# Performance work log

Hardware: AMD Instinct MI355X
Metric: run time of the kernel (lower is better)

## Reference

```python
import jax, jax.numpy as jnp
import numpy as np

N_NODES = 50000
N_REL = 8
N_EDGES = 64000
D_IN = 128
D_OUT = 128


def setup_inputs() -> dict:
    key = jax.random.key(0)
    k1, k2, k3, k4 = jax.random.split(key, 4)
    features = jax.random.normal(k1, (N_NODES, D_IN), dtype=jnp.float32)
    W = jax.random.normal(k2, (N_REL, D_IN, D_OUT), dtype=jnp.float32) * 0.05
    b = jnp.zeros((N_REL, D_OUT), dtype=jnp.float32)
    src = jax.random.randint(k3, (N_REL, N_EDGES), 0, N_NODES, dtype=jnp.int64)
    dst = jax.random.randint(k4, (N_REL, N_EDGES), 0, N_NODES, dtype=jnp.int64)
    return {"features": features, "W": W, "b": b, "src": src, "dst": dst}


def reference(features, W, b, src, dst):
    # R-GCN layer: per-relation DGL GraphConv (norm='both', bias) summed over relations.
    N = features.shape[0]
    R = W.shape[0]
    out = jnp.zeros((N, W.shape[-1]), dtype=features.dtype)
    for r in range(R):  # fixed small relation count; edges fully vectorized
        s, d = src[r], dst[r]
        ones = jnp.ones(s.shape[0], dtype=features.dtype)
        out_deg = jnp.clip(jax.ops.segment_sum(ones, s, num_segments=N), 1.0)
        in_deg = jnp.clip(jax.ops.segment_sum(ones, d, num_segments=N), 1.0)
        # pre-scale source features by out_degree^-1/2, gather, aggregate to dst
        m = features * (out_deg ** -0.5)[:, None]          # [N, D_in]
        agg = jax.ops.segment_sum(m[s], d, num_segments=N)  # [N, D_in]
        # weight after aggregation (in_feats == out_feats path), then dst norm + bias
        rst = (agg @ W[r]) * (in_deg ** -0.5)[:, None] + b[r]
        out = out + rst  # HeteroGraphConv aggregate='sum'
    return out
```

## Files before the change

kernel.cpp:

```cpp
#include <hip/hip_runtime.h>

#define N_NODES 50000
#define N_REL 8
#define N_EDGES 64000
#define D 128
#define TROWS 32
#define NT 1563
#define CAP 128
#define SLABW 66
#define GRID 521

typedef __attribute__((ext_vector_type(8))) short short8;
typedef __attribute__((ext_vector_type(4))) float f32x4;

__device__ __forceinline__ unsigned short f2bf(float x) {
  unsigned int u = __float_as_uint(x);
  u += 0x7FFFu + ((u >> 16) & 1u);
  return (unsigned short)(u >> 16);
}
__device__ __forceinline__ float bflo(unsigned v) { return __uint_as_float(v << 16); }
__device__ __forceinline__ float bfhi(unsigned v) { return __uint_as_float(v & 0xFFFF0000u); }
__device__ __forceinline__ unsigned packbf(float x, float y) {
  return (unsigned)f2bf(x) | ((unsigned)f2bf(y) << 16);
}

__global__ __launch_bounds__(256) void setup_kernel(
    const int* __restrict__ src, const int* __restrict__ dst,
    const float* __restrict__ F, const float* __restrict__ W,
    const float* __restrict__ b, int* __restrict__ outc, int* __restrict__ inc,
    uint2* __restrict__ F16, unsigned short* __restrict__ Wt,
    float* __restrict__ bs) {
  int bid = blockIdx.x, t = threadIdx.x;
  if (bid < 2000) {
    int i = bid * 256 + t;
    int r = i / N_EDGES;
    atomicAdd(&outc[r * N_NODES + src[i]], 1);
    atomicAdd(&inc[r * N_NODES + dst[i]], 1);
  } else if (bid < 8250) {
    int i = (bid - 2000) * 256 + t;
    float4 v = ((const float4*)F)[i];
    uint2 o;
    o.x = packbf(v.x, v.y);
    o.y = packbf(v.z, v.w);
    F16[i] = o;
  } else {
    int i = (bid - 8250) * 256 + t;
    int r = i >> 14, rem = i & 16383, n = rem >> 7, k = rem & 127;
    Wt[i] = f2bf(W[(r << 14) + (k << 7) + n]);
    if (bid == 8250 && t < D) {
      float v = 0.f;
#pragma unroll
      for (int rr = 0; rr < N_REL; ++rr) v += b[rr * D + t];
      bs[t] = v;
    }
  }
}

__global__ __launch_bounds__(256) void bucket_kernel(
    const int* __restrict__ src, const int* __restrict__ dst,
    const int* __restrict__ outc, const int* __restrict__ inc,
    int* __restrict__ bcnt, int2* __restrict__ buckets) {
  int i = blockIdx.x * 256 + threadIdx.x;
  int r = i / N_EDGES;
  int s = src[i], d = dst[i];
  float c = rsqrtf(fmaxf((float)outc[r * N_NODES + s], 1.0f)) *
            rsqrtf(fmaxf((float)inc[r * N_NODES + d], 1.0f));
  int tile = d >> 5;
  int slot = atomicAdd(&bcnt[r * NT + tile], 1);
  if (slot < CAP)
    buckets[(size_t)(r * NT + tile) * CAP + slot] =
        make_int2(s | ((d & 31) << 17), __float_as_int(c));
}

__global__ __launch_bounds__(512, 2) void fused_kernel(
    const unsigned int* __restrict__ F16,
    const unsigned short* __restrict__ Wt,
    const int* __restrict__ bcnt,
    const int2* __restrict__ buckets,
    const float* __restrict__ bs,
    float* __restrict__ out) {
  __shared__ unsigned slabs[8][TROWS * SLABW];
  __shared__ int2 dlds[8][CAP];
  int tid = threadIdx.x;
  int lane = tid & 63;
  int w = __builtin_amdgcn_readfirstlane(tid >> 6);
  int l15 = lane & 15, g = lane >> 4;

  short8 bfr[8][4];
#pragma unroll
  for (int r = 0; r < 8; ++r)
#pragma unroll
    for (int ks = 0; ks < 4; ++ks)
      bfr[r][ks] = *(const short8*)&Wt[(size_t)r * D * D +
                                       (w * 16 + l15) * D + ks * 32 + g * 8];
  float bias = bs[w * 16 + l15];

#define RMW(dd, fv)                                           \
  {                                                           \
    int row_ = ((dd).x >> 17) & 31;                           \
    unsigned* p_ = &slabs[w][row_ * SLABW + lane];            \
    float c_ = __int_as_float((dd).y);                        \
    unsigned old_ = *p_;                                      \
    float vx_ = fmaf(c_, bflo(fv), bflo(old_));               \
    float vy_ = fmaf(c_, bfhi(fv), bfhi(old_));               \
    *p_ = packbf(vx_, vy_);                                   \
  }

  for (int t = blockIdx.x; t < NT; t += GRID) {
    __syncthreads();

    for (int i = lane; i < TROWS * SLABW; i += 64) slabs[w][i] = 0u;

    int n = min(bcnt[w * NT + t], CAP);
    const int2* bk = &buckets[(size_t)(w * NT + t) * CAP];
    if (lane < n) dlds[w][lane] = bk[lane];
    if (lane + 64 < n) dlds[w][lane + 64] = bk[lane + 64];

    int i = 0;
    for (; i + 4 <= n; i += 4) {
      int2 d0 = dlds[w][i], d1 = dlds[w][i + 1], d2 = dlds[w][i + 2],
           d3 = dlds[w][i + 3];
      unsigned f0 = F16[(unsigned)(d0.x & 0x1FFFF) * 64 + lane];
      unsigned f1 = F16[(unsigned)(d1.x & 0x1FFFF) * 64 + lane];
      unsigned f2 = F16[(unsigned)(d2.x & 0x1FFFF) * 64 + lane];
      unsigned f3 = F16[(unsigned)(d3.x & 0x1FFFF) * 64 + lane];
      RMW(d0, f0) RMW(d1, f1) RMW(d2, f2) RMW(d3, f3)
    }
    for (; i < n; ++i) {
      int2 dd = dlds[w][i];
      unsigned fv = F16[(unsigned)(dd.x & 0x1FFFF) * 64 + lane];
      RMW(dd, fv)
    }

    __syncthreads();

    f32x4 a0 = (f32x4){0.f, 0.f, 0.f, 0.f};
    f32x4 a1 = (f32x4){0.f, 0.f, 0.f, 0.f};
#pragma unroll
    for (int r = 0; r < 8; ++r) {
#pragma unroll
      for (int ks = 0; ks < 4; ++ks) {
        short8 A0 = *(const short8*)&slabs[r][l15 * SLABW + ks * 16 + g * 4];
        short8 A1 =
            *(const short8*)&slabs[r][(16 + l15) * SLABW + ks * 16 + g * 4];
        a0 = __builtin_amdgcn_mfma_f32_16x16x32_bf16(A0, bfr[r][ks], a0, 0, 0, 0);
        a1 = __builtin_amdgcn_mfma_f32_16x16x32_bf16(A1, bfr[r][ks], a1, 0, 0, 0);
      }
    }

    int t0 = t * TROWS;
    int col = w * 16 + l15;
#pragma unroll
    for (int q = 0; q < 4; ++q) {
      int row0 = t0 + g * 4 + q;
      if (row0 < N_NODES) out[(size_t)row0 * D + col] = a0[q] + bias;
      int row1 = t0 + 16 + g * 4 + q;
      if (row1 < N_NODES) out[(size_t)row1 * D + col] = a1[q] + bias;
    }
  }
#undef RMW
}

extern "C" void kernel_launch(void* const* d_in, const int* in_sizes, int n_in,
                              void* d_out, int out_size, void* d_ws, size_t ws_size,
                              hipStream_t stream) {
  const float* F = (const float*)d_in[0];
  const float* W = (const float*)d_in[1];
  const float* b = (const float*)d_in[2];
  const int* src = (const int*)d_in[3];
  const int* dst = (const int*)d_in[4];
  float* out = (float*)d_out;

  char* ws = (char*)d_ws;
  size_t o = 0;
  int* outc = (int*)(ws + o);  o += (size_t)N_REL * N_NODES * 4;
  int* inc = (int*)(ws + o);   o += (size_t)N_REL * N_NODES * 4;
  int* bcnt = (int*)(ws + o);  o += (size_t)N_REL * NT * 4;
  size_t zero_bytes = o;
  int2* buckets = (int2*)(ws + o);               o += (size_t)N_REL * NT * CAP * 8;
  unsigned int* F16 = (unsigned int*)(ws + o);   o += (size_t)N_NODES * 64 * 4;
  unsigned short* Wt = (unsigned short*)(ws + o); o += (size_t)N_REL * D * D * 2;
  float* bs = (float*)(ws + o);                  o += D * 4;

  hipMemsetAsync(outc, 0, zero_bytes, stream);
  setup_kernel<<<8762, 256, 0, stream>>>(src, dst, F, W, b, outc, inc,
                                         (uint2*)F16, Wt, bs);
  bucket_kernel<<<2000, 256, 0, stream>>>(src, dst, outc, inc, bcnt, buckets);
  fused_kernel<<<GRID, 512, 0, stream>>>(F16, Wt, bcnt, buckets, bs, out);
}
```

Before: 207.6 us.

## Merge memset, setup, bucket and fused kernels into one cooperative kernel

Replaces the memset plus three kernel launches with a single cooperative kernel that uses grid-wide syncs between the zeroing, degree counting and conversion, bucketing, and aggregate/GEMM phases. The goal is to remove launch gaps and per-kernel tail overhead. In exchange, the grid shrinks to 256 blocks, so the fused phase runs with fewer blocks and has to pay for grid.sync barriers and the cooperative launch. The Wt conversion covers exactly 131072 threads, which matches N_REL*D*D.

```diff
diff --git a/kernel.cpp b/kernel.cpp
--- a/kernel.cpp
+++ b/kernel.cpp
@@ -1,4 +1,7 @@
 #include <hip/hip_runtime.h>
+#include <hip/hip_cooperative_groups.h>
+
+namespace cg = cooperative_groups;
 
 #define N_NODES 50000
 #define N_REL 8
@@ -8,7 +11,8 @@
 #define NT 1563
 #define CAP 128
 #define SLABW 66
-#define GRID 521
+#define GRID 256
+#define NTHR (GRID * 512)
 
 typedef __attribute__((ext_vector_type(8))) short short8;
 typedef __attribute__((ext_vector_type(4))) float f32x4;
@@ -24,64 +28,59 @@
   return (unsigned)f2bf(x) | ((unsigned)f2bf(y) << 16);
 }
 
-__global__ __launch_bounds__(256) void setup_kernel(
+__global__ __launch_bounds__(512, 2) void mega_kernel(
     const int* __restrict__ src, const int* __restrict__ dst,
     const float* __restrict__ F, const float* __restrict__ W,
     const float* __restrict__ b, int* __restrict__ outc, int* __restrict__ inc,
-    uint2* __restrict__ F16, unsigned short* __restrict__ Wt,
-    float* __restrict__ bs) {
-  int bid = blockIdx.x, t = threadIdx.x;
-  if (bid < 2000) {
-    int i = bid * 256 + t;
-    int r = i / N_EDGES;
-    atomicAdd(&outc[r * N_NODES + src[i]], 1);
-    atomicAdd(&inc[r * N_NODES + dst[i]], 1);
-  } else if (bid < 8250) {
-    int i = (bid - 2000) * 256 + t;
-    float4 v = ((const float4*)F)[i];
-    uint2 o;
-    o.x = packbf(v.x, v.y);
-    o.y = packbf(v.z, v.w);
-    F16[i] = o;
-  } else {
-    int i = (bid - 8250) * 256 + t;
-    int r = i >> 14, rem = i & 16383, n = rem >> 7, k = rem & 127;
-    Wt[i] = f2bf(W[(r << 14) + (k << 7) + n]);
-    if (bid == 8250 && t < D) {
-      float v = 0.f;
-#pragma unroll
-      for (int rr = 0; rr < N_REL; ++rr) v += b[rr * D + t];
-      bs[t] = v;
-    }
-  }
-}
-
-__global__ __launch_bounds__(256) void bucket_kernel(
-    const int* __restrict__ src, const int* __restrict__ dst,
-    const int* __restrict__ outc, const int* __restrict__ inc,
-    int* __restrict__ bcnt, int2* __restrict__ buckets) {
-  int i = blockIdx.x * 256 + threadIdx.x;
-  int r = i / N_EDGES;
-  int s = src[i], d = dst[i];
-  float c = rsqrtf(fmaxf((float)outc[r * N_NODES + s], 1.0f)) *
-            rsqrtf(fmaxf((float)inc[r * N_NODES + d], 1.0f));
-  int tile = d >> 5;
-  int slot = atomicAdd(&bcnt[r * NT + tile], 1);
-  if (slot < CAP)
-    buckets[(size_t)(r * NT + tile) * CAP + slot] =
-        make_int2(s | ((d & 31) << 17), __float_as_int(c));
-}
-
-__global__ __launch_bounds__(512, 2) void fused_kernel(
-    const unsigned int* __restrict__ F16,
-    const unsigned short* __restrict__ Wt,
-    const int* __restrict__ bcnt,
-    const int2* __restrict__ buckets,
-    const float* __restrict__ bs,
-    float* __restrict__ out) {
+    int* __restrict__ bcnt, int2* __restrict__ buckets,
+    unsigned* __restrict__ F16, unsigned short* __restrict__ Wt,
+    float* __restrict__ bs, float* __restrict__ out) {
+  cg::grid_group grid = cg::this_grid();
   __shared__ unsigned slabs[8][TROWS * SLABW];
   __shared__ int2 dlds[8][CAP];
   int tid = threadIdx.x;
+  int gtid = blockIdx.x * 512 + tid;
+
+  const int ZWORDS = 2 * N_REL * N_NODES + N_REL * NT;
+  for (int i = gtid; i < ZWORDS; i += NTHR) outc[i] = 0;
+  grid.sync();
+
+  for (int e = gtid; e < N_REL * N_EDGES; e += NTHR) {
+    int r = e / N_EDGES;
+    atomicAdd(&outc[r * N_NODES + src[e]], 1);
+    atomicAdd(&inc[r * N_NODES + dst[e]], 1);
+  }
+  {
+    const float4* F4 = (const float4*)F;
+    for (int i = gtid; i < N_NODES * 32; i += NTHR) {
+      float4 v = F4[i];
+      ((uint2*)F16)[i] = make_uint2(packbf(v.x, v.y), packbf(v.z, v.w));
+    }
+    int i = gtid;
+    int r = i >> 14, rem = i & 16383, n = rem >> 7, k = rem & 127;
+    Wt[i] = f2bf(W[(r << 14) + (k << 7) + n]);
+    if (gtid < D) {
+      float v = 0.f;
+#pragma unroll
+      for (int rr = 0; rr < N_REL; ++rr) v += b[rr * D + gtid];
+      bs[gtid] = v;
+    }
+  }
+  grid.sync();
+
+  for (int e = gtid; e < N_REL * N_EDGES; e += NTHR) {
+    int r = e / N_EDGES;
+    int s = src[e], d = dst[e];
+    float c = rsqrtf(fmaxf((float)outc[r * N_NODES + s], 1.0f)) *
+              rsqrtf(fmaxf((float)inc[r * N_NODES + d], 1.0f));
+    int tile = d >> 5;
+    int slot = atomicAdd(&bcnt[r * NT + tile], 1);
+    if (slot < CAP)
+      buckets[(size_t)(r * NT + tile) * CAP + slot] =
+          make_int2(s | ((d & 31) << 17), __float_as_int(c));
+  }
+  grid.sync();
+
   int lane = tid & 63;
   int w = __builtin_amdgcn_readfirstlane(tid >> 6);
   int l15 = lane & 15, g = lane >> 4;
@@ -164,11 +163,11 @@
 extern "C" void kernel_launch(void* const* d_in, const int* in_sizes, int n_in,
                               void* d_out, int out_size, void* d_ws, size_t ws_size,
                               hipStream_t stream) {
+  const int* src = (const int*)d_in[3];
+  const int* dst = (const int*)d_in[4];
   const float* F = (const float*)d_in[0];
   const float* W = (const float*)d_in[1];
   const float* b = (const float*)d_in[2];
-  const int* src = (const int*)d_in[3];
-  const int* dst = (const int*)d_in[4];
   float* out = (float*)d_out;
 
   char* ws = (char*)d_ws;
@@ -176,15 +175,15 @@
   int* outc = (int*)(ws + o);  o += (size_t)N_REL * N_NODES * 4;
   int* inc = (int*)(ws + o);   o += (size_t)N_REL * N_NODES * 4;
   int* bcnt = (int*)(ws + o);  o += (size_t)N_REL * NT * 4;
-  size_t zero_bytes = o;
-  int2* buckets = (int2*)(ws + o);               o += (size_t)N_REL * NT * CAP * 8;
-  unsigned int* F16 = (unsigned int*)(ws + o);   o += (size_t)N_NODES * 64 * 4;
+  int2* buckets = (int2*)(ws + o);                o += (size_t)N_REL * NT * CAP * 8;
+  unsigned* F16 = (unsigned*)(ws + o);            o += (size_t)N_NODES * 64 * 4;
   unsigned short* Wt = (unsigned short*)(ws + o); o += (size_t)N_REL * D * D * 2;
-  float* bs = (float*)(ws + o);                  o += D * 4;
+  float* bs = (float*)(ws + o);                   o += D * 4;
 
-  hipMemsetAsync(outc, 0, zero_bytes, stream);
-  setup_kernel<<<8762, 256, 0, stream>>>(src, dst, F, W, b, outc, inc,
-                                         (uint2*)F16, Wt, bs);
-  bucket_kernel<<<2000, 256, 0, stream>>>(src, dst, outc, inc, bcnt, buckets);
-  fused_kernel<<<GRID, 512, 0, stream>>>(F16, Wt, bcnt, buckets, bs, out);
+  void* args[] = {(void*)&src, (void*)&dst, (void*)&F,    (void*)&W,
+                  (void*)&b,   (void*)&outc, (void*)&inc, (void*)&bcnt,
+                  (void*)&buckets, (void*)&F16, (void*)&Wt, (void*)&bs,
+                  (void*)&out};
+  hipLaunchCooperativeKernel((void*)mega_kernel, dim3(GRID), dim3(512), args, 0,
+                             stream);
 }
```

New measurement: 267.6 us. 1.29x slower.
